# Performance work log

Measured on AMD Instinct MI355X. Metric: run time of the kernel, lower is better.

Reference implementation:

```python
import jax, jax.numpy as jnp
import numpy as np
import math

D_MODEL = 1024
N = 64
TAU_MIN = 1e-4

def _next_pow_two(n: int) -> int:
    return 1 << (n - 1).bit_length()

def setup_inputs() -> dict:
    key = jax.random.key(0)
    ks = jax.random.split(key, 6)
    Bb, T = 4, 8192
    half = N // 2
    n = jnp.arange(half, dtype=jnp.float32)
    x = jax.random.normal(ks[0], (Bb, T, D_MODEL), dtype=jnp.float32)
    log_tau = jnp.full((half,), math.log(0.5), dtype=jnp.float32)
    freq = (math.pi * (2 * n + 1) / 2).astype(jnp.float32)  # hippoD init
    Bp = 1.0 + 0.2 * jax.random.normal(ks[1], (half,), dtype=jnp.float32)
    Cp = (1.0 / math.sqrt(half)) * jax.random.normal(ks[2], (half,), dtype=jnp.float32)
    log_dt = jnp.zeros((), dtype=jnp.float32)
    # torch Linear weight layout: (out_features, in_features)
    W_in = jax.random.normal(ks[3], (half, D_MODEL), dtype=jnp.float32) / math.sqrt(D_MODEL)
    W_out = jax.random.normal(ks[4], (D_MODEL, half), dtype=jnp.float32) / math.sqrt(half)
    return {"x": x, "log_tau": log_tau, "freq": freq, "Bp": Bp, "Cp": Cp,
            "log_dt": log_dt, "W_in": W_in, "W_out": W_out}

def reference(x, log_tau, freq, Bp, Cp, log_dt, W_in, W_out):
    Bb, T, _ = x.shape
    L = _next_pow_two(2 * T)  # static
    half = log_tau.shape[0]
    # ---- analytic kernel (N, T) ----
    dt = jnp.exp(log_dt)
    tau = jnp.clip(jnp.exp(log_tau), TAU_MIN)
    angle = freq * dt                       # (half,)
    log_lam_mag = -tau * dt                 # log of exp(-tau*dt)
    log_gain = jnp.log(jnp.abs(Bp) + 1e-9) + jnp.log(jnp.abs(Cp) + 1e-9)
    i = jnp.arange(T, dtype=x.dtype)
    amp = jnp.exp(log_gain[:, None] + i[None, :] * log_lam_mag[:, None])  # (half, T)
    K_half = amp * jnp.cos(i[None, :] * angle[:, None])                   # (half, T)
    K_full = jnp.concatenate([K_half, K_half[::-1]], axis=0)              # (N, T)
    Kf = jnp.fft.rfft(K_full, n=L, axis=-1)                               # (N, L//2+1)
    # ---- FFT convolution ----
    x_proj = jnp.einsum('btd,nd->btn', x, W_in)                           # (B,T,half)
    x_modes = jnp.concatenate([x_proj, x_proj[..., ::-1]], axis=-1)       # (B,T,N)
    Uf = jnp.fft.rfft(x_modes, n=L, axis=1).transpose(0, 2, 1)            # (B,N,L//2+1)
    Yf = Uf * Kf[None]
    y_modes = jnp.fft.irfft(Yf, n=L, axis=2)[..., :T].transpose(0, 2, 1)  # (B,T,N)
    y = y_modes[..., :half]                                               # (B,T,half)
    return jnp.einsum('btn,dn->btd', y, W_out)
```

## Files before the change

kernel.cpp:

```cpp
#include <hip/hip_runtime.h>
#include <math.h>

#define NB 4
#define TT 8192
#define DM 1024
#define NH 32
#define CT 64
#define NG (TT/CT)
#define DK 128
#define MW 4

__global__ __launch_bounds__(512, 4) void k1_proj_scan(
    const float* __restrict__ x, const float* __restrict__ Wi,
    const float* __restrict__ log_tau, const float* __restrict__ freq,
    const float* __restrict__ log_dt,
    float2* __restrict__ hl, float2* __restrict__ Ech)
{
    __shared__ float xs[CT * 129];
    __shared__ float ws[NH * DK];
    const int c    = blockIdx.x;
    const int b    = blockIdx.y;
    const int t0   = c * CT;
    const int tid  = threadIdx.x;
    const int lane = tid & 63;
    const int wv   = tid >> 6;

    float acc[MW] = {0.f, 0.f, 0.f, 0.f};
    const float* xb = x + ((size_t)b * TT + t0) * DM;

    for (int dk = 0; dk < DM; dk += DK) {
#pragma unroll
        for (int it = 0; it < 4; ++it) {
            int idx4 = tid + it * 512;
            int tt   = idx4 >> 5;
            int cc   = idx4 & 31;
            float4 v = *(const float4*)(xb + (size_t)tt * DM + dk + cc * 4);
            float vv[4] = {v.x, v.y, v.z, v.w};
            float* p = &xs[tt * 129 + cc * 4];
            int q = (idx4 >> 3) & 3;
#pragma unroll
            for (int k = 0; k < 4; ++k) { int j = (k + q) & 3; p[j] = vv[j]; }
        }
#pragma unroll
        for (int it = 0; it < 2; ++it) {
            int idx4 = tid + it * 512;
            int nn   = idx4 >> 5;
            int d4   = (idx4 & 31) * 4;
            *(float4*)(&ws[nn * DK + d4]) =
                *(const float4*)(Wi + (size_t)nn * DM + dk + d4);
        }
        __syncthreads();
#pragma unroll 4
        for (int d4 = 0; d4 < DK; d4 += 4) {
            const float* xr = &xs[lane * 129 + d4];
            float x0 = xr[0], x1 = xr[1], x2 = xr[2], x3 = xr[3];
#pragma unroll
            for (int j = 0; j < MW; ++j) {
                const float4 w = *(const float4*)(&ws[(wv * MW + j) * DK + d4]);
                acc[j] = fmaf(x3, w.w, fmaf(x2, w.z, fmaf(x1, w.y, fmaf(x0, w.x, acc[j]))));
            }
        }
        __syncthreads();
    }

    const float dtv = expf(log_dt[0]);
#pragma unroll
    for (int j = 0; j < MW; ++j) {
        const int n = wv * MW + j;
        const float tau = fmaxf(expf(log_tau[n]), 1e-4f);
        const float rr  = expf(-tau * dtv);
        const float th  = freq[n] * dtv;
        float pr = rr * cosf(th), pi = rr * sinf(th);
        float vr = acc[j], vi = 0.f;
#pragma unroll
        for (int off = 1; off < 64; off <<= 1) {
            float ur = __shfl_up(vr, (unsigned)off);
            float ui = __shfl_up(vi, (unsigned)off);
            if (lane >= off) {
                vr = fmaf(pr, ur, fmaf(-pi, ui, vr));
                vi = fmaf(pr, ui, fmaf( pi, ur, vi));
            }
            float sr = pr * pr - pi * pi;
            float si = 2.f * pr * pi;
            pr = sr; pi = si;
        }
        hl[((size_t)(b * NG + c) * NH + n) * CT + lane] = make_float2(vr, vi);
        if (lane == 63) {
            Ech[((size_t)b * NH + n) * NG + c] = make_float2(vr, vi);
        }
    }
}

__global__ __launch_bounds__(256) void k2_chunkscan(
    const float* __restrict__ log_tau, const float* __restrict__ freq,
    const float* __restrict__ log_dt,
    const float2* __restrict__ Ech, float2* __restrict__ Hin)
{
    const int b    = blockIdx.x;
    const int lane = threadIdx.x & 63;
    const int wv   = threadIdx.x >> 6;
    const double dtv = exp((double)log_dt[0]);
#pragma unroll
    for (int j = 0; j < 8; ++j) {
        const int n = wv * 8 + j;
        const double tau = fmax(exp((double)log_tau[n]), 1e-4);
        const double a   = (double)freq[n] * dtv * (double)CT;
        const double m   = exp(-tau * dtv * (double)CT);
        const float Lr = (float)(m * cos(a));
        const float Li = (float)(m * sin(a));
        const float2* eb = Ech + ((size_t)b * NH + n) * NG;
        float2 e0 = eb[2 * lane];
        float2 e1 = eb[2 * lane + 1];
        float vr = fmaf(Lr, e0.x, fmaf(-Li, e0.y, e1.x));
        float vi = fmaf(Lr, e0.y, fmaf( Li, e0.x, e1.y));
        float pr = Lr * Lr - Li * Li;
        float pi = 2.f * Lr * Li;
#pragma unroll
        for (int off = 1; off < 64; off <<= 1) {
            float ur = __shfl_up(vr, (unsigned)off);
            float ui = __shfl_up(vi, (unsigned)off);
            if (lane >= off) {
                vr = fmaf(pr, ur, fmaf(-pi, ui, vr));
                vi = fmaf(pr, ui, fmaf( pi, ur, vi));
            }
            float sr = pr * pr - pi * pi;
            float si = 2.f * pr * pi;
            pr = sr; pi = si;
        }
        float wr = __shfl_up(vr, 1u), wi = __shfl_up(vi, 1u);
        if (lane == 0) { wr = 0.f; wi = 0.f; }
        float2* hb = Hin + ((size_t)b * NH + n) * NG;
        hb[2 * lane]     = make_float2(wr, wi);
        hb[2 * lane + 1] = make_float2(fmaf(Lr, wr, fmaf(-Li, wi, e0.x)),
                                       fmaf(Lr, wi, fmaf( Li, wr, e0.y)));
    }
}

__global__ __launch_bounds__(512, 4) void k3_out(
    const float2* __restrict__ hl, const float2* __restrict__ Hin,
    const float* __restrict__ Wo,
    const float* __restrict__ log_tau, const float* __restrict__ freq,
    const float* __restrict__ Bp, const float* __restrict__ Cp,
    const float* __restrict__ log_dt,
    float* __restrict__ out)
{
    __shared__ float ysT[NH * 64];
    __shared__ float wT[NH * 513];
    const int c    = blockIdx.x;
    const int b    = blockIdx.y;
    const int t0   = c * CT;
    const int tid  = threadIdx.x;
    const int lane = tid & 63;
    const int wv   = tid >> 6;

    {
        const float dtv = expf(log_dt[0]);
        const int t = lane;
#pragma unroll
        for (int j = 0; j < 4; ++j) {
            const int n = wv * 4 + j;
            const float tau = fmaxf(expf(log_tau[n]), 1e-4f);
            const float rr  = expf(-tau * dtv);
            const float th  = freq[n] * dtv;
            const float g   = (fabsf(Bp[n]) + 1e-9f) * (fabsf(Cp[n]) + 1e-9f);
            float p2r = rr * cosf(th), p2i = rr * sinf(th);
            float pwr = 1.f, pwi = 0.f;
            const int e = t + 1;
#pragma unroll
            for (int bit = 0; bit < 7; ++bit) {
                if (e & (1 << bit)) {
                    float nr = pwr * p2r - pwi * p2i;
                    float ni = pwr * p2i + pwi * p2r;
                    pwr = nr; pwi = ni;
                }
                float sr = p2r * p2r - p2i * p2i;
                float si = 2.f * p2r * p2i;
                p2r = sr; p2i = si;
            }
            float2 hv = hl[((size_t)(b * NG + c) * NH + n) * CT + t];
            float2 Hv = Hin[((size_t)b * NH + n) * NG + c];
            ysT[n * 64 + t] = g * (hv.x + pwr * Hv.x - pwi * Hv.y);
        }
    }

    const int qd = wv >> 2;
    const int tg = wv & 3;
    const int dbase = qd * 256 + lane;
    float* const outb = out + ((size_t)b * TT + t0) * DM;
    for (int db = 0; db < DM; db += 512) {
        __syncthreads();
#pragma unroll
        for (int it = 0; it < 32; ++it) {
            int idx = tid + it * 512;
            int dl  = idx >> 5;
            int nn  = idx & 31;
            wT[nn * 513 + dl] = Wo[(size_t)(db + dl) * NH + nn];
        }
        __syncthreads();
        float a0[16], a1[16], a2[16], a3[16];
#pragma unroll
        for (int i = 0; i < 16; ++i) { a0[i] = a1[i] = a2[i] = a3[i] = 0.f; }
#pragma unroll 4
        for (int n = 0; n < NH; ++n) {
            const float w0 = wT[n * 513 + dbase];
            const float w1 = wT[n * 513 + dbase + 64];
            const float w2 = wT[n * 513 + dbase + 128];
            const float w3 = wT[n * 513 + dbase + 192];
            const float* yr = &ysT[n * 64 + tg * 16];
#pragma unroll
            for (int i = 0; i < 16; ++i) {
                const float yv = yr[i];
                a0[i] = fmaf(yv, w0, a0[i]);
                a1[i] = fmaf(yv, w1, a1[i]);
                a2[i] = fmaf(yv, w2, a2[i]);
                a3[i] = fmaf(yv, w3, a3[i]);
            }
        }
#pragma unroll
        for (int i = 0; i < 16; ++i) {
            float* op = outb + (size_t)(tg * 16 + i) * DM + db + dbase;
            op[0]   = a0[i];
            op[64]  = a1[i];
            op[128] = a2[i];
            op[192] = a3[i];
        }
    }
}

extern "C" void kernel_launch(void* const* d_in, const int* in_sizes, int n_in,
                              void* d_out, int out_size, void* d_ws, size_t ws_size,
                              hipStream_t stream)
{
    (void)in_sizes; (void)n_in; (void)out_size; (void)ws_size;
    const float* x       = (const float*)d_in[0];
    const float* log_tau = (const float*)d_in[1];
    const float* freq    = (const float*)d_in[2];
    const float* Bp      = (const float*)d_in[3];
    const float* Cp      = (const float*)d_in[4];
    const float* log_dt  = (const float*)d_in[5];
    const float* Wi      = (const float*)d_in[6];
    const float* Wo      = (const float*)d_in[7];
    float* out = (float*)d_out;

    float2* hl  = (float2*)d_ws;
    float2* Ech = hl  + (size_t)NB * NG * NH * CT;
    float2* Hin = Ech + (size_t)NB * NH * NG;

    dim3 grid(NG, NB);
    k1_proj_scan<<<grid, 512, 0, stream>>>(x, Wi, log_tau, freq, log_dt, hl, Ech);
    k2_chunkscan<<<NB, 256, 0, stream>>>(log_tau, freq, log_dt, Ech, Hin);
    k3_out<<<grid, 512, 0, stream>>>(hl, Hin, Wo, log_tau, freq, Bp, Cp, log_dt, out);
}
```

Baseline: 313.7 us.

## Split-K projection with async double-buffered LDS loads and cross-wave reduction

Rewrites the input projection in the first kernel. Each wave now takes a slice of every 128-wide d-chunk and accumulates all 32 modes per thread, with W_in read straight from global memory at wave-uniform addresses. The chunks of x are staged into XOR-swizzled LDS through double-buffered global_load_lds, so loads overlap compute without a padded layout. A final LDS reduction across the 8 waves rebuilds per-mode sums before the scan. This raises register pressure (32 accumulators per thread) and relies on the async LDS loads completing correctly before each barrier.

```diff
diff --git a/kernel.cpp b/kernel.cpp
--- a/kernel.cpp
+++ b/kernel.cpp
@@ -10,57 +10,90 @@
 #define DK 128
 #define MW 4
 
+__device__ __forceinline__ void gload_lds16(const float* g, float* l)
+{
+    __builtin_amdgcn_global_load_lds(
+        (const __attribute__((address_space(1))) void*)g,
+        (__attribute__((address_space(3))) void*)l, 16, 0, 0);
+}
+
 __global__ __launch_bounds__(512, 4) void k1_proj_scan(
     const float* __restrict__ x, const float* __restrict__ Wi,
     const float* __restrict__ log_tau, const float* __restrict__ freq,
     const float* __restrict__ log_dt,
     float2* __restrict__ hl, float2* __restrict__ Ech)
 {
-    __shared__ float xs[CT * 129];
-    __shared__ float ws[NH * DK];
+    __shared__ float xs[2][CT * DK];
     const int c    = blockIdx.x;
     const int b    = blockIdx.y;
     const int t0   = c * CT;
     const int tid  = threadIdx.x;
     const int lane = tid & 63;
     const int wv   = tid >> 6;
-
-    float acc[MW] = {0.f, 0.f, 0.f, 0.f};
+    const int wvs  = __builtin_amdgcn_readfirstlane(wv);
+    const int l7   = lane & 7;
+
     const float* xb = x + ((size_t)b * TT + t0) * DM;
 
-    for (int dk = 0; dk < DM; dk += DK) {
-#pragma unroll
-        for (int it = 0; it < 4; ++it) {
-            int idx4 = tid + it * 512;
-            int tt   = idx4 >> 5;
-            int cc   = idx4 & 31;
-            float4 v = *(const float4*)(xb + (size_t)tt * DM + dk + cc * 4);
-            float vv[4] = {v.x, v.y, v.z, v.w};
-            float* p = &xs[tt * 129 + cc * 4];
-            int q = (idx4 >> 3) & 3;
-#pragma unroll
-            for (int k = 0; k < 4; ++k) { int j = (k + q) & 3; p[j] = vv[j]; }
-        }
-#pragma unroll
-        for (int it = 0; it < 2; ++it) {
-            int idx4 = tid + it * 512;
-            int nn   = idx4 >> 5;
-            int d4   = (idx4 & 31) * 4;
-            *(float4*)(&ws[nn * DK + d4]) =
-                *(const float4*)(Wi + (size_t)nn * DM + dk + d4);
+    float acc[NH];
+#pragma unroll
+    for (int n = 0; n < NH; ++n) acc[n] = 0.f;
+
+    const int sr0 = (wv << 3) + (lane >> 5);
+    const int sc0 = lane & 31;
+
+#pragma unroll
+    for (int i = 0; i < 4; ++i) {
+        const int r  = sr0 + (i << 1);
+        const int cc = sc0 ^ (r & 7);
+        gload_lds16(xb + (size_t)r * DM + (cc << 2),
+                    &xs[0][0] + (((wvs << 3) + (i << 1)) * DK));
+    }
+    __syncthreads();
+
+    for (int ck = 0; ck < DM / DK; ++ck) {
+        if (ck + 1 < DM / DK) {
+            float* dst = &xs[(ck + 1) & 1][0] + ((wvs << 3) * DK);
+#pragma unroll
+            for (int i = 0; i < 4; ++i) {
+                const int r  = sr0 + (i << 1);
+                const int cc = sc0 ^ (r & 7);
+                gload_lds16(xb + (size_t)r * DM + (size_t)(ck + 1) * DK + (cc << 2),
+                            dst + (i << 1) * DK);
+            }
+        }
+        const char*  xrow = (const char*)(&xs[ck & 1][0]) + lane * (DK * 4);
+        const float* wch  = Wi + ck * DK;
+#pragma unroll
+        for (int s = 0; s < 4; ++s) {
+            const int g = (wvs << 2) + s;
+            const float4 xv = *(const float4*)(xrow + ((g ^ l7) << 4));
+            const float* wp = wch + (g << 2);
+#pragma unroll
+            for (int n = 0; n < NH; ++n) {
+                const float4 w4 = *(const float4*)(wp + (size_t)n * DM);
+                acc[n] = fmaf(xv.w, w4.w, fmaf(xv.z, w4.z,
+                         fmaf(xv.y, w4.y, fmaf(xv.x, w4.x, acc[n]))));
+            }
         }
         __syncthreads();
-#pragma unroll 4
-        for (int d4 = 0; d4 < DK; d4 += 4) {
-            const float* xr = &xs[lane * 129 + d4];
-            float x0 = xr[0], x1 = xr[1], x2 = xr[2], x3 = xr[3];
-#pragma unroll
-            for (int j = 0; j < MW; ++j) {
-                const float4 w = *(const float4*)(&ws[(wv * MW + j) * DK + d4]);
-                acc[j] = fmaf(x3, w.w, fmaf(x2, w.z, fmaf(x1, w.y, fmaf(x0, w.x, acc[j]))));
-            }
-        }
-        __syncthreads();
+    }
+
+    float* red = (float*)xs;
+#pragma unroll
+    for (int n = 0; n < NH; ++n)
+        red[(wv << 11) + (n << 6) + lane] = acc[n];
+    __syncthreads();
+
+    float am[MW];
+#pragma unroll
+    for (int j = 0; j < MW; ++j) {
+        const int n = wv * MW + j;
+        float s = 0.f;
+#pragma unroll
+        for (int w = 0; w < 8; ++w)
+            s += red[(w << 11) + (n << 6) + lane];
+        am[j] = s;
     }
 
     const float dtv = expf(log_dt[0]);
@@ -71,7 +104,7 @@
         const float rr  = expf(-tau * dtv);
         const float th  = freq[n] * dtv;
         float pr = rr * cosf(th), pi = rr * sinf(th);
-        float vr = acc[j], vi = 0.f;
+        float vr = am[j], vi = 0.f;
 #pragma unroll
         for (int off = 1; off < 64; off <<= 1) {
             float ur = __shfl_up(vr, (unsigned)off);
```

Result: slower. 343.6 us (+9.5%).
